# Performance work log

Measured on AMD Instinct MI355X. Metric: run time of the kernel, lower is better.

The kernel has to match this reference:

```python
import jax, jax.numpy as jnp
import numpy as np

N_INST, N_PERS, N_PROD = 20000, 50000, 30000
E_INST, E_PERS, E_PROD = 160000, 400000, 240000
F_IN, HID, HEADS, OUT = 128, 64, 4, 2
D = HID * HEADS  # 256
NEG_SLOPE_ATT = 0.2   # GATv2 attention leaky-relu slope
NEG_SLOPE_ACT = 0.01  # F.leaky_relu default
BN_EPS = 1e-5


def gatv2(x, src, dst, Wl, Wr, att, b, N):
    """Single-relation GATv2Conv (concat heads, add_self_loops=True)."""
    loop = jnp.arange(N, dtype=src.dtype)
    s = jnp.concatenate([src, loop])
    d = jnp.concatenate([dst, loop])
    H, C = att.shape
    hl = (x @ Wl).reshape(N, H, C)  # source transform
    hr = (x @ Wr).reshape(N, H, C)  # target transform
    e = jax.nn.leaky_relu(hl[s] + hr[d], NEG_SLOPE_ATT)        # [E,H,C]
    score = jnp.einsum('ehc,hc->eh', e, att)                   # [E,H]
    mx = jax.lax.stop_gradient(jax.ops.segment_max(score, d, num_segments=N))
    ex = jnp.exp(score - mx[d])
    den = jax.ops.segment_sum(ex, d, num_segments=N)           # [N,H]
    alpha = ex / (den[d] + 1e-16)
    out = jax.ops.segment_sum(alpha[..., None] * hl[s], d, num_segments=N)
    return out.reshape(N, H * C) + b


def batchnorm(x, g, b):
    mu = jnp.mean(x, axis=0)
    var = jnp.var(x, axis=0)
    return (x - mu) * jax.lax.rsqrt(var + BN_EPS) * g + b


def setup_inputs() -> dict:
    key = jax.random.key(0)
    ks = jax.random.split(key, 16)
    s = 0.05
    return {
        'x_inst': jax.random.normal(ks[0], (N_INST, F_IN), jnp.float32),
        'x_pers': jax.random.normal(ks[1], (N_PERS, F_IN), jnp.float32),
        'x_prod': jax.random.normal(ks[2], (N_PROD, F_IN), jnp.float32),
        'ei_inst': jax.random.randint(ks[3], (2, E_INST), 0, N_INST, jnp.int32),
        'ei_pers': jax.random.randint(ks[4], (2, E_PERS), 0, N_PERS, jnp.int32),
        'ei_prod': jax.random.randint(ks[5], (2, E_PROD), 0, N_PROD, jnp.int32),
        'Wl1': jax.random.normal(ks[6], (3, F_IN, D), jnp.float32) * s,
        'Wr1': jax.random.normal(ks[7], (3, F_IN, D), jnp.float32) * s,
        'att1': jax.random.normal(ks[8], (3, HEADS, HID), jnp.float32) * s,
        'b1': jnp.zeros((3, D), jnp.float32),
        'Wl2': jax.random.normal(ks[9], (3, D, D), jnp.float32) * s,
        'Wr2': jax.random.normal(ks[10], (3, D, D), jnp.float32) * s,
        'att2': jax.random.normal(ks[11], (3, HEADS, HID), jnp.float32) * s,
        'b2': jnp.zeros((3, D), jnp.float32),
        'bn_g': jnp.ones((3, D), jnp.float32),
        'bn_b': jnp.zeros((3, D), jnp.float32),
        'cW': jax.random.normal(ks[12], (D, OUT), jnp.float32) * s,
        'cb': jnp.zeros((OUT,), jnp.float32),
    }


def reference(x_inst, x_pers, x_prod, ei_inst, ei_pers, ei_prod,
              Wl1, Wr1, att1, b1, Wl2, Wr2, att2, b2,
              bn_g, bn_b, cW, cb):
    xs = (x_inst, x_pers, x_prod)
    eis = (ei_inst, ei_pers, ei_prod)
    outs = []
    for i in range(3):  # fixed set of node types
        x = xs[i]
        N = x.shape[0]
        src, dst = eis[i][0], eis[i][1]
        h = gatv2(x, src, dst, Wl1[i], Wr1[i], att1[i], b1[i], N)
        h = jax.nn.leaky_relu(batchnorm(h, bn_g[i], bn_b[i]), NEG_SLOPE_ACT)
        h = gatv2(h, src, dst, Wl2[i], Wr2[i], att2[i], b2[i], N)
        h = jax.nn.leaky_relu(batchnorm(h, bn_g[i], bn_b[i]), NEG_SLOPE_ACT)
        outs.append(h @ cW + cb)
    return tuple(outs)
```

## Files before the change

kernel.cpp:

```cpp
#include <hip/hip_runtime.h>

#define DFEAT 256
#define NEG_ATT 0.2f
#define NEG_ACT 0.01f
#define BN_EPS 1e-5f

typedef short bf16x8 __attribute__((ext_vector_type(8)));
typedef float f32x4 __attribute__((ext_vector_type(4)));

struct Int3 { int a[3]; };
struct Cp3 { const void* p[3]; };
struct Vp3 { void* p[3]; };
struct WJobs { const float* src[12]; unsigned short* dst[12]; int K[12]; };

__device__ __forceinline__ float lrelu(float x, float s) { return x > 0.f ? x : s * x; }

__device__ __forceinline__ unsigned short f2bf(float f) {
    union { float f; unsigned int u; } v; v.f = f;
    unsigned int u = v.u;
    unsigned int r = (u + 0x7FFFu + ((u >> 16) & 1u)) >> 16;
    return (unsigned short)r;
}
__device__ __forceinline__ float bf2f(unsigned short s) {
    union { unsigned int u; float f; } v; v.u = ((unsigned int)s) << 16;
    return v.f;
}
__device__ __forceinline__ float u_lo(unsigned u) {
    union { unsigned u; float f; } v; v.u = u << 16; return v.f;
}
__device__ __forceinline__ float u_hi(unsigned u) {
    union { unsigned u; float f; } v; v.u = u & 0xffff0000u; return v.f;
}

__global__ __launch_bounds__(256)
void hist_all_k(Cp3 dst, Int3 E, int* __restrict__ counts_all, Int3 nodeOff) {
    int t = blockIdx.y;
    int e = blockIdx.x * 256 + threadIdx.x;
    if (e >= E.a[t]) return;
    const int* dstp = (const int*)dst.p[t];
    atomicAdd(&counts_all[nodeOff.a[t] + dstp[e]], 1);
}

__global__ __launch_bounds__(256)
void scan1_all_k(const int* __restrict__ counts_all, int* __restrict__ offs_all,
                 int* __restrict__ bsums_all, Int3 N, Int3 nodeOff, Int3 bOff) {
    int t = blockIdx.y;
    if (blockIdx.x * 256 >= N.a[t]) return;
    const int* counts = counts_all + nodeOff.a[t];
    int* offs = offs_all + nodeOff.a[t] + t;
    int* bsums = bsums_all + bOff.a[t];
    __shared__ int buf[256];
    int tt = threadIdx.x;
    int i = blockIdx.x * 256 + tt;
    int v = (i < N.a[t]) ? counts[i] : 0;
    buf[tt] = v;
    __syncthreads();
    for (int off = 1; off < 256; off <<= 1) {
        int x = (tt >= off) ? buf[tt - off] : 0;
        __syncthreads();
        buf[tt] += x;
        __syncthreads();
    }
    if (i < N.a[t]) offs[i] = buf[tt];
    if (tt == 255) bsums[blockIdx.x] = buf[255];
}

__global__ __launch_bounds__(256)
void scan2_all_k(int* __restrict__ bsums_all, Int3 N, Int3 bOff) {
    int t = blockIdx.x;
    int nb = (N.a[t] + 255) / 256;
    int* bsums = bsums_all + bOff.a[t];
    __shared__ int buf[256];
    __shared__ int carry_s;
    int tt = threadIdx.x;
    if (tt == 0) carry_s = 0;
    __syncthreads();
    for (int base = 0; base < nb; base += 256) {
        int i = base + tt;
        int v = (i < nb) ? bsums[i] : 0;
        buf[tt] = v;
        __syncthreads();
        for (int off = 1; off < 256; off <<= 1) {
            int x = (tt >= off) ? buf[tt - off] : 0;
            __syncthreads();
            buf[tt] += x;
            __syncthreads();
        }
        int incl = buf[tt];
        int c = carry_s;
        if (i < nb) bsums[i] = c + incl - v;
        __syncthreads();
        if (tt == 255) carry_s = c + buf[255];
        __syncthreads();
    }
}

__global__ __launch_bounds__(256)
void scan3_all_k(int* __restrict__ offs_all, const int* __restrict__ counts_all,
                 const int* __restrict__ bsums_all, Int3 N, Int3 E,
                 Int3 nodeOff, Int3 bOff) {
    int t = blockIdx.y;
    if (blockIdx.x * 256 >= N.a[t]) return;
    int* offs = offs_all + nodeOff.a[t] + t;
    const int* counts = counts_all + nodeOff.a[t];
    const int* bsums = bsums_all + bOff.a[t];
    int i = blockIdx.x * 256 + threadIdx.x;
    if (i < N.a[t]) offs[i] = offs[i] - counts[i] + bsums[blockIdx.x];
    if (i == 0) offs[N.a[t]] = E.a[t];
}

__global__ __launch_bounds__(256)
void scatter_all_k(Cp3 src, Cp3 dst, Int3 E, const int* __restrict__ offs_all,
                   int* __restrict__ counts_all, int* __restrict__ csr_all,
                   Int3 nodeOff, Int3 edgeOff) {
    int t = blockIdx.y;
    int e = blockIdx.x * 256 + threadIdx.x;
    if (e >= E.a[t]) return;
    const int* srcp = (const int*)src.p[t];
    const int* dstp = (const int*)dst.p[t];
    const int* offs = offs_all + nodeOff.a[t] + t;
    int* cursor = counts_all + nodeOff.a[t];
    int* csr = csr_all + edgeOff.a[t];
    int d = dstp[e];
    int pos = atomicSub(&cursor[d], 1) - 1;
    csr[offs[d] + pos] = srcp[e];
}

__global__ __launch_bounds__(256)
void wcast_tr_k(WJobs jobs) {
    int j = blockIdx.z;
    int K = jobs.K[j];
    int k0 = blockIdx.y * 64;
    if (k0 >= K) return;
    int n0 = blockIdx.x * 64;
    const float* W = jobs.src[j];
    unsigned short* Bt = jobs.dst[j];
    __shared__ float tile[64][65];
    int tid = threadIdx.x;
    int tr = tid >> 4;
    int tc4 = (tid & 15) << 2;
#pragma unroll
    for (int r = 0; r < 4; ++r) {
        int k = tr + r * 16;
        float4 v = *(const float4*)(W + (size_t)(k0 + k) * 256 + n0 + tc4);
        tile[k][tc4] = v.x; tile[k][tc4 + 1] = v.y;
        tile[k][tc4 + 2] = v.z; tile[k][tc4 + 3] = v.w;
    }
    __syncthreads();
    int n = tid >> 2;
    int kc = (tid & 3) << 4;
    unsigned o[8];
#pragma unroll
    for (int q = 0; q < 8; ++q) {
        float v0 = tile[kc + 2 * q][n];
        float v1 = tile[kc + 2 * q + 1][n];
        o[q] = (unsigned)f2bf(v0) | ((unsigned)f2bf(v1) << 16);
    }
    unsigned short* dp = Bt + (size_t)(n0 + n) * K + k0 + kc;
    *(uint4*)dp = make_uint4(o[0], o[1], o[2], o[3]);
    *(uint4*)(dp + 8) = make_uint4(o[4], o[5], o[6], o[7]);
}

template<int AMODE>
__global__ __launch_bounds__(256)
void mfma_gemm_all_k(Cp3 Ap3, Cp3 Bp3, Cp3 ssP, Vp3 Cp3v, Int3 M3, int K) {
    int t = blockIdx.z;
    int M = M3.a[t];
    int bm = blockIdx.x * 128;
    if (bm >= M) return;
    const void* Ap = Ap3.p[t];
    const unsigned short* Bt = (const unsigned short*)Bp3.p[t];
    const float* ss = (const float*)ssP.p[t];
    unsigned short* C = (unsigned short*)Cp3v.p[t];
    const int LDK = 40;
    __shared__ unsigned short As[128 * LDK];
    __shared__ unsigned short Bs[128 * LDK];
    int tid = threadIdx.x;
    int bn = blockIdx.y * 128;
    int wid = tid >> 6, lane = tid & 63;
    int quad = lane >> 4, l16 = lane & 15;
    int mw = (wid & 1) * 64, nw = (wid >> 1) * 64;
    f32x4 acc[4][4] = {};
    for (int k0 = 0; k0 < K; k0 += 32) {
#pragma unroll
        for (int i = 0; i < 2; ++i) {
            int c = tid + 256 * i;
            int row = c >> 2, ko = (c & 3) * 8;
            int ra = bm + row; if (ra >= M) ra = M - 1;
            if (AMODE == 1) {
                const float* Af = (const float*)Ap;
                float4 a0 = *(const float4*)(Af + (size_t)ra * K + k0 + ko);
                float4 a1 = *(const float4*)(Af + (size_t)ra * K + k0 + ko + 4);
                ushort4 lo, hi;
                lo.x = f2bf(a0.x); lo.y = f2bf(a0.y); lo.z = f2bf(a0.z); lo.w = f2bf(a0.w);
                hi.x = f2bf(a1.x); hi.y = f2bf(a1.y); hi.z = f2bf(a1.z); hi.w = f2bf(a1.w);
                *(ushort4*)&As[row * LDK + ko] = lo;
                *(ushort4*)&As[row * LDK + ko + 4] = hi;
            } else if (AMODE == 2) {
                const unsigned short* Ab = (const unsigned short*)Ap;
                uint4 va = *(const uint4*)(Ab + (size_t)ra * K + k0 + ko);
                const unsigned* up = (const unsigned*)&va;
                float4 sc0 = *(const float4*)(ss + k0 + ko);
                float4 sc1 = *(const float4*)(ss + k0 + ko + 4);
                float4 sh0 = *(const float4*)(ss + 256 + k0 + ko);
                float4 sh1 = *(const float4*)(ss + 256 + k0 + ko + 4);
                float fv[8] = {u_lo(up[0]), u_hi(up[0]), u_lo(up[1]), u_hi(up[1]),
                               u_lo(up[2]), u_hi(up[2]), u_lo(up[3]), u_hi(up[3])};
                float scv[8] = {sc0.x, sc0.y, sc0.z, sc0.w, sc1.x, sc1.y, sc1.z, sc1.w};
                float shv[8] = {sh0.x, sh0.y, sh0.z, sh0.w, sh1.x, sh1.y, sh1.z, sh1.w};
                unsigned ov[4];
#pragma unroll
                for (int q = 0; q < 4; ++q) {
                    float v0 = fmaf(fv[2 * q], scv[2 * q], shv[2 * q]);
                    v0 = fmaxf(v0, NEG_ACT * v0);
                    float v1 = fmaf(fv[2 * q + 1], scv[2 * q + 1], shv[2 * q + 1]);
                    v1 = fmaxf(v1, NEG_ACT * v1);
                    ov[q] = (unsigned)f2bf(v0) | ((unsigned)f2bf(v1) << 16);
                }
                *(uint4*)&As[row * LDK + ko] = make_uint4(ov[0], ov[1], ov[2], ov[3]);
            } else {
                const unsigned short* Ab = (const unsigned short*)Ap;
                uint4 va = *(const uint4*)(Ab + (size_t)ra * K + k0 + ko);
                *(uint4*)&As[row * LDK + ko] = va;
            }
            uint4 vb = *(const uint4*)(Bt + (size_t)(bn + row) * K + k0 + ko);
            *(uint4*)&Bs[row * LDK + ko] = vb;
        }
        __syncthreads();
        bf16x8 af[4], bfv[4];
#pragma unroll
        for (int i = 0; i < 4; ++i)
            af[i] = *(bf16x8*)&As[(mw + 16 * i + l16) * LDK + quad * 8];
#pragma unroll
        for (int u = 0; u < 4; ++u)
            bfv[u] = *(bf16x8*)&Bs[(nw + 16 * u + l16) * LDK + quad * 8];
#pragma unroll
        for (int i = 0; i < 4; ++i)
#pragma unroll
            for (int u = 0; u < 4; ++u)
                acc[i][u] = __builtin_amdgcn_mfma_f32_16x16x32_bf16(af[i], bfv[u], acc[i][u], 0, 0, 0);
        __syncthreads();
    }
#pragma unroll
    for (int i = 0; i < 4; ++i) {
#pragma unroll
        for (int r = 0; r < 4; ++r) {
            int grow = bm + mw + 16 * i + quad * 4 + r;
            if (grow < M) {
#pragma unroll
                for (int u = 0; u < 4; ++u) {
                    int gcol = bn + nw + 16 * u + l16;
                    C[(size_t)grow * 512 + gcol] = f2bf(acc[i][u][r]);
                }
            }
        }
    }
}

__global__ __launch_bounds__(256, 8)
void gat_gather_all_k(Cp3 hl3, Cp3 offs3, Cp3 csr3, Cp3 att3, Cp3 bias3,
                      Vp3 out3, Int3 N3) {
    int t = blockIdx.z;
    int N = N3.a[t];
    int wave = (blockIdx.x * 256 + threadIdx.x) >> 6;
    int lane = threadIdx.x & 63;
    if (wave >= N) return;
    int d = wave;
    int half = lane >> 5;
    int l32 = lane & 31;
    const char* hlB = (const char*)hl3.p[t];
    const int* offs = (const int*)offs3.p[t];
    const int* csr  = (const int*)csr3.p[t];
    const float* att  = (const float*)att3.p[t];
    const float* bias = (const float*)bias3.p[t];
    unsigned short* out = (unsigned short*)out3.p[t];

    unsigned fOff = (unsigned)l32 << 4;

    float hr[8], at[8], ac[8];
    {
        uint4 u = *(const uint4*)(hlB + (((unsigned)d << 10) + 512u + fOff));
        const unsigned* up = (const unsigned*)&u;
#pragma unroll
        for (int j = 0; j < 4; ++j) { hr[2 * j] = u_lo(up[j]); hr[2 * j + 1] = u_hi(up[j]); }
        const float4* ap = (const float4*)(att + (l32 << 3));
        float4 a0 = ap[0], a1 = ap[1];
        at[0] = a0.x; at[1] = a0.y; at[2] = a0.z; at[3] = a0.w;
        at[4] = a1.x; at[5] = a1.y; at[6] = a1.z; at[7] = a1.w;
    }
#pragma unroll
    for (int j = 0; j < 8; ++j) ac[j] = 0.f;
    float lsum = 0.f;

    auto pair_update = [&](uint4 u, bool active) {
        const unsigned* up = (const unsigned*)&u;
        float h[8];
#pragma unroll
        for (int j = 0; j < 4; ++j) { h[2 * j] = u_lo(up[j]); h[2 * j + 1] = u_hi(up[j]); }
        float part = 0.f;
#pragma unroll
        for (int j = 0; j < 8; ++j) {
            float x = h[j] + hr[j];
            x = fmaxf(x, NEG_ATT * x);
            part = fmaf(x, at[j], part);
        }
        part += __shfl_xor(part, 1);
        part += __shfl_xor(part, 2);
        part += __shfl_xor(part, 4);
        float p = active ? __expf(part) : 0.f;
        lsum += p;
#pragma unroll
        for (int j = 0; j < 8; ++j) ac[j] = fmaf(p, h[j], ac[j]);
    };

    pair_update(*(const uint4*)(hlB + (((unsigned)d << 10) + fOff)), half == 0);

    int beg = offs[d];
    int deg = offs[d + 1] - beg;
    for (int base = 0; base < deg; base += 64) {
        int cnt = min(64, deg - base);
        int my = (base + lane < deg) ? csr[beg + base + lane] : d;
        for (int j = 0; j < cnt; j += 6) {
            uint4 v[3];
#pragma unroll
            for (int u = 0; u < 3; ++u) {
                int ei = j + 2 * u + half;
                int s = __shfl(my, ei & 63);
                if (j + 2 * u < cnt) v[u] = *(const uint4*)(hlB + (((unsigned)s << 10) + fOff));
            }
#pragma unroll
            for (int u = 0; u < 3; ++u)
                if (j + 2 * u < cnt) pair_update(v[u], (j + 2 * u + half) < cnt);
        }
    }

    lsum += __shfl_xor(lsum, 32);
#pragma unroll
    for (int j = 0; j < 8; ++j) ac[j] += __shfl_xor(ac[j], 32);

    if (half == 0) {
        float inv = 1.f / (lsum + 1e-16f);
        const float4* bp = (const float4*)(bias + (l32 << 3));
        float4 b0 = bp[0], b1 = bp[1];
        float bb[8] = {b0.x, b0.y, b0.z, b0.w, b1.x, b1.y, b1.z, b1.w};
        unsigned o[4];
#pragma unroll
        for (int j = 0; j < 4; ++j) {
            float v0 = fmaf(ac[2 * j], inv, bb[2 * j]);
            float v1 = fmaf(ac[2 * j + 1], inv, bb[2 * j + 1]);
            o[j] = (unsigned)f2bf(v0) | ((unsigned)f2bf(v1) << 16);
        }
        *(uint4*)((char*)out + (((unsigned)d << 9) + fOff)) = make_uint4(o[0], o[1], o[2], o[3]);
    }
}

__global__ __launch_bounds__(256)
void bn_stats_all_k(Cp3 h3, Vp3 st3, Int3 N3) {
    int t = blockIdx.y;
    const unsigned short* hp = (const unsigned short*)h3.p[t];
    float* st = (float*)st3.p[t];
    long total = (long)N3.a[t] * 256;
    int tid = threadIdx.x;
    long gt = (long)blockIdx.x * 256 + tid;
    long stride = (long)gridDim.x * 256 * 8;
    float s[8] = {0.f}, s2[8] = {0.f};
    for (long p = gt * 8; p < total; p += stride) {
        uint4 u = *(const uint4*)(hp + p);
        unsigned short* us = (unsigned short*)&u;
#pragma unroll
        for (int j = 0; j < 8; ++j) { float v = bf2f(us[j]); s[j] += v; s2[j] += v * v; }
    }
#pragma unroll
    for (int j = 0; j < 8; ++j) { s[j] += __shfl_xor(s[j], 32); s2[j] += __shfl_xor(s2[j], 32); }
    __shared__ float lds[2048];
    int wv = tid >> 6, lane = tid & 63;
    if (lane < 32) {
#pragma unroll
        for (int j = 0; j < 8; ++j) {
            lds[wv * 512 + lane * 8 + j] = s[j];
            lds[wv * 512 + 256 + lane * 8 + j] = s2[j];
        }
    }
    __syncthreads();
    for (int q = tid; q < 512; q += 256) {
        float v = lds[q] + lds[512 + q] + lds[1024 + q] + lds[1536 + q];
        atomicAdd(&st[q], v);
    }
}

__global__ __launch_bounds__(256)
void bn_finalize_all_k(Cp3 st3, const float* __restrict__ gb, const float* __restrict__ bb,
                       Vp3 ss3, Int3 N3) {
    int t = blockIdx.x;
    const float* st = (const float*)st3.p[t];
    float* ss = (float*)ss3.p[t];
    int f = threadIdx.x;
    float invN = 1.f / (float)N3.a[t];
    float mu  = st[f] * invN;
    float var = st[256 + f] * invN - mu * mu;
    float sc  = gb[t * DFEAT + f] / sqrtf(var + BN_EPS);
    ss[f] = sc;
    ss[256 + f] = bb[t * DFEAT + f] - mu * sc;
}

__global__ __launch_bounds__(256)
void bn_cls_all_k(Cp3 R3, Cp3 st3, const float* __restrict__ gb, const float* __restrict__ bb,
                  const float* __restrict__ cW, const float* __restrict__ cb,
                  Vp3 out3, Int3 N3) {
    int t = blockIdx.y;
    int N = N3.a[t];
    int wave = (blockIdx.x * 256 + threadIdx.x) >> 6;
    int lane = threadIdx.x & 63;
    if (wave >= N) return;
    const unsigned short* R = (const unsigned short*)R3.p[t];
    const float* stats = (const float*)st3.p[t];
    const float* g = gb + (size_t)t * DFEAT;
    const float* b = bb + (size_t)t * DFEAT;
    float* out = (float*)out3.p[t];
    int f4 = lane << 2;
    float invN = 1.f / (float)N;
    ushort4 u = *(const ushort4*)(R + (size_t)wave * DFEAT + f4);
    float vv[4] = {bf2f(u.x), bf2f(u.y), bf2f(u.z), bf2f(u.w)};
    float p0 = 0.f, p1 = 0.f;
#pragma unroll
    for (int j = 0; j < 4; ++j) {
        int f = f4 + j;
        float mu  = stats[f] * invN;
        float var = stats[DFEAT + f] * invN - mu * mu;
        float sc  = g[f] / sqrtf(var + BN_EPS);
        float val = lrelu((vv[j] - mu) * sc + b[f], NEG_ACT);
        float2 w = *(const float2*)(cW + (size_t)f * 2);
        p0 += val * w.x;
        p1 += val * w.y;
    }
#pragma unroll
    for (int off = 1; off < 64; off <<= 1) {
        p0 += __shfl_xor(p0, off);
        p1 += __shfl_xor(p1, off);
    }
    if (lane == 0) {
        out[(size_t)wave * 2 + 0] = p0 + cb[0];
        out[(size_t)wave * 2 + 1] = p1 + cb[1];
    }
}

extern "C" void kernel_launch(void* const* d_in, const int* in_sizes, int n_in,
                              void* d_out, int out_size, void* d_ws, size_t ws_size,
                              hipStream_t stream) {
    const float* x0 = (const float*)d_in[0];
    const float* x1 = (const float*)d_in[1];
    const float* x2 = (const float*)d_in[2];
    const int* ei[3] = {(const int*)d_in[3], (const int*)d_in[4], (const int*)d_in[5]};
    const float* Wl1 = (const float*)d_in[6];
    const float* Wr1 = (const float*)d_in[7];
    const float* att1 = (const float*)d_in[8];
    const float* b1 = (const float*)d_in[9];
    const float* Wl2 = (const float*)d_in[10];
    const float* Wr2 = (const float*)d_in[11];
    const float* att2 = (const float*)d_in[12];
    const float* b2 = (const float*)d_in[13];
    const float* bn_g = (const float*)d_in[14];
    const float* bn_b = (const float*)d_in[15];
    const float* cW = (const float*)d_in[16];
    const float* cb = (const float*)d_in[17];

    Int3 N3, E3, nodeOff, edgeOff, bOff;
    N3.a[0] = in_sizes[0] / 128; N3.a[1] = in_sizes[1] / 128; N3.a[2] = in_sizes[2] / 128;
    E3.a[0] = in_sizes[3] / 2;   E3.a[1] = in_sizes[4] / 2;   E3.a[2] = in_sizes[5] / 2;
    int Ntot = 0, Etot = 0, btot = 0;
    int maxN = 0, maxE = 0;
    for (int i = 0; i < 3; ++i) {
        nodeOff.a[i] = Ntot; edgeOff.a[i] = Etot; bOff.a[i] = btot;
        Ntot += N3.a[i]; Etot += E3.a[i]; btot += (N3.a[i] + 255) / 256;
        if (N3.a[i] > maxN) maxN = N3.a[i];
        if (E3.a[i] > maxE) maxE = E3.a[i];
    }

    char* w = (char*)d_ws;
    auto alloc_b = [&](size_t bytes) -> void* {
        void* p = (void*)w;
        w += (bytes + 255) & ~(size_t)255;
        return p;
    };
    unsigned short* C_all  = (unsigned short*)alloc_b((size_t)Ntot * 512 * sizeof(unsigned short));
    unsigned short* Rb_all = (unsigned short*)alloc_b((size_t)Ntot * DFEAT * sizeof(unsigned short));
    unsigned short* Bt1 = (unsigned short*)alloc_b((size_t)3 * 512 * 128 * sizeof(unsigned short));
    unsigned short* Bt2 = (unsigned short*)alloc_b((size_t)3 * 512 * 256 * sizeof(unsigned short));
    int* counts_all = (int*)alloc_b((size_t)Ntot * sizeof(int));
    int* offs_all   = (int*)alloc_b((size_t)(Ntot + 3) * sizeof(int));
    int* csr_all    = (int*)alloc_b((size_t)Etot * sizeof(int));
    int* bsums_all  = (int*)alloc_b((size_t)btot * sizeof(int));
    float* stats_all = (float*)alloc_b((size_t)6 * 512 * sizeof(float));
    float* ss_all    = (float*)alloc_b((size_t)3 * 512 * sizeof(float));

    Cp3 srcP, dstP, xP, Bt1P, Bt2P, hlP, offsP, csrP, att1P, att2P, b1P, b2P;
    Cp3 RbCP, st1CP, st2CP, ssCP, dumP;
    Vp3 CP, RbP, st1P, st2P, ssP, outP;
    for (int i = 0; i < 3; ++i) {
        srcP.p[i] = ei[i];
        dstP.p[i] = ei[i] + E3.a[i];
        xP.p[i] = (i == 0) ? (const void*)x0 : (i == 1) ? (const void*)x1 : (const void*)x2;
        Bt1P.p[i] = Bt1 + (size_t)i * 512 * 128;
        Bt2P.p[i] = Bt2 + (size_t)i * 512 * 256;
        CP.p[i] = C_all + (size_t)nodeOff.a[i] * 512;
        hlP.p[i] = CP.p[i];
        RbP.p[i] = Rb_all + (size_t)nodeOff.a[i] * DFEAT;
        RbCP.p[i] = RbP.p[i];
        offsP.p[i] = offs_all + nodeOff.a[i] + i;
        csrP.p[i] = csr_all + edgeOff.a[i];
        att1P.p[i] = att1 + (size_t)i * DFEAT;
        att2P.p[i] = att2 + (size_t)i * DFEAT;
        b1P.p[i] = b1 + (size_t)i * DFEAT;
        b2P.p[i] = b2 + (size_t)i * DFEAT;
        st1P.p[i] = stats_all + (size_t)i * 512;
        st2P.p[i] = stats_all + (size_t)(3 + i) * 512;
        st1CP.p[i] = st1P.p[i];
        st2CP.p[i] = st2P.p[i];
        ssP.p[i] = ss_all + (size_t)i * 512;
        ssCP.p[i] = ssP.p[i];
        dumP.p[i] = xP.p[i];
        outP.p[i] = (float*)d_out + (size_t)nodeOff.a[i] * 2;
    }

    int maxNblk = (maxN + 255) / 256;
    int maxEblk = (maxE + 255) / 256;
    int maxMtile = (maxN + 127) / 128;
    int maxNwave = (maxN + 3) / 4;

    hipMemsetAsync(counts_all, 0, (size_t)Ntot * sizeof(int), stream);
    hipMemsetAsync(stats_all, 0, (size_t)6 * 512 * sizeof(float), stream);
    {
        WJobs jobs;
        for (int i = 0; i < 3; ++i) {
            jobs.src[i * 4 + 0] = Wl1 + (size_t)i * 128 * 256;
            jobs.dst[i * 4 + 0] = (unsigned short*)Bt1P.p[i];
            jobs.K[i * 4 + 0] = 128;
            jobs.src[i * 4 + 1] = Wr1 + (size_t)i * 128 * 256;
            jobs.dst[i * 4 + 1] = (unsigned short*)Bt1P.p[i] + (size_t)256 * 128;
            jobs.K[i * 4 + 1] = 128;
            jobs.src[i * 4 + 2] = Wl2 + (size_t)i * 256 * 256;
            jobs.dst[i * 4 + 2] = (unsigned short*)Bt2P.p[i];
            jobs.K[i * 4 + 2] = 256;
            jobs.src[i * 4 + 3] = Wr2 + (size_t)i * 256 * 256;
            jobs.dst[i * 4 + 3] = (unsigned short*)Bt2P.p[i] + (size_t)256 * 256;
            jobs.K[i * 4 + 3] = 256;
        }
        wcast_tr_k<<<dim3(4, 4, 12), 256, 0, stream>>>(jobs);
    }

    hist_all_k<<<dim3(maxEblk, 3), 256, 0, stream>>>(dstP, E3, counts_all, nodeOff);
    scan1_all_k<<<dim3(maxNblk, 3), 256, 0, stream>>>(counts_all, offs_all, bsums_all, N3, nodeOff, bOff);
    scan2_all_k<<<3, 256, 0, stream>>>(bsums_all, N3, bOff);
    scan3_all_k<<<dim3(maxNblk, 3), 256, 0, stream>>>(offs_all, counts_all, bsums_all, N3, E3, nodeOff, bOff);
    scatter_all_k<<<dim3(maxEblk, 3), 256, 0, stream>>>(srcP, dstP, E3, offs_all, counts_all, csr_all, nodeOff, edgeOff);

    mfma_gemm_all_k<1><<<dim3(maxMtile, 4, 3), 256, 0, stream>>>(xP, Bt1P, dumP, CP, N3, 128);
    gat_gather_all_k<<<dim3(maxNwave, 1, 3), 256, 0, stream>>>(hlP, offsP, csrP, att1P, b1P, RbP, N3);
    bn_stats_all_k<<<dim3(512, 3), 256, 0, stream>>>(RbCP, st1P, N3);
    bn_finalize_all_k<<<3, 256, 0, stream>>>(st1CP, bn_g, bn_b, ssP, N3);

    mfma_gemm_all_k<2><<<dim3(maxMtile, 4, 3), 256, 0, stream>>>(RbCP, Bt2P, ssCP, CP, N3, 256);
    gat_gather_all_k<<<dim3(maxNwave, 1, 3), 256, 0, stream>>>(hlP, offsP, csrP, att2P, b2P, RbP, N3);
    bn_stats_all_k<<<dim3(512, 3), 256, 0, stream>>>(RbCP, st2P, N3);

    bn_cls_all_k<<<dim3(maxNwave, 3), 256, 0, stream>>>(RbCP, st2CP, bn_g, bn_b, cW, cb, outP, N3);
}
```

Baseline: 642.3 us.

## Map one edge per full wave with 4 features per lane in GAT gather

The GATv2 gather kernel now handles one edge per full wave, each lane covering 4 bf16 features with 8-byte loads. Before, each half-wave handled its own edge with 16-byte loads. Neighbour loads are batched 8 at a time, with a separate masked tail, instead of 3 pair-loads. The aim is more loads in flight, less half-wave masking at the tail, and no cross-half reduction at the end. The cost is an extra shuffle step in the per-head reduction and narrower memory transactions per lane; dropping the occupancy hint from launch bounds may also change register allocation.

```diff
diff --git a/kernel.cpp b/kernel.cpp
--- a/kernel.cpp
+++ b/kernel.cpp
@@ -257,7 +257,7 @@
     }
 }
 
-__global__ __launch_bounds__(256, 8)
+__global__ __launch_bounds__(256)
 void gat_gather_all_k(Cp3 hl3, Cp3 offs3, Cp3 csr3, Cp3 att3, Cp3 bias3,
                       Vp3 out3, Int3 N3) {
     int t = blockIdx.z;
@@ -265,93 +265,79 @@
     int wave = (blockIdx.x * 256 + threadIdx.x) >> 6;
     int lane = threadIdx.x & 63;
     if (wave >= N) return;
-    int d = wave;
-    int half = lane >> 5;
-    int l32 = lane & 31;
     const char* hlB = (const char*)hl3.p[t];
     const int* offs = (const int*)offs3.p[t];
-    const int* csr  = (const int*)csr3.p[t];
-    const float* att  = (const float*)att3.p[t];
+    const int* csr = (const int*)csr3.p[t];
+    const float* att = (const float*)att3.p[t];
     const float* bias = (const float*)bias3.p[t];
     unsigned short* out = (unsigned short*)out3.p[t];
-
-    unsigned fOff = (unsigned)l32 << 4;
-
-    float hr[8], at[8], ac[8];
-    {
-        uint4 u = *(const uint4*)(hlB + (((unsigned)d << 10) + 512u + fOff));
-        const unsigned* up = (const unsigned*)&u;
-#pragma unroll
-        for (int j = 0; j < 4; ++j) { hr[2 * j] = u_lo(up[j]); hr[2 * j + 1] = u_hi(up[j]); }
-        const float4* ap = (const float4*)(att + (l32 << 3));
-        float4 a0 = ap[0], a1 = ap[1];
-        at[0] = a0.x; at[1] = a0.y; at[2] = a0.z; at[3] = a0.w;
-        at[4] = a1.x; at[5] = a1.y; at[6] = a1.z; at[7] = a1.w;
-    }
-#pragma unroll
-    for (int j = 0; j < 8; ++j) ac[j] = 0.f;
-    float lsum = 0.f;
-
-    auto pair_update = [&](uint4 u, bool active) {
-        const unsigned* up = (const unsigned*)&u;
-        float h[8];
-#pragma unroll
-        for (int j = 0; j < 4; ++j) { h[2 * j] = u_lo(up[j]); h[2 * j + 1] = u_hi(up[j]); }
-        float part = 0.f;
-#pragma unroll
-        for (int j = 0; j < 8; ++j) {
-            float x = h[j] + hr[j];
-            x = fmaxf(x, NEG_ATT * x);
-            part = fmaf(x, at[j], part);
-        }
+    int d = wave;
+    unsigned lOff = (unsigned)lane << 3;
+    ushort4 hru = *(const ushort4*)(hlB + (((unsigned)d << 10) + 512u + lOff));
+    float hr0 = bf2f(hru.x), hr1 = bf2f(hru.y), hr2 = bf2f(hru.z), hr3 = bf2f(hru.w);
+    float4 av  = *(const float4*)(att + (lane << 2));
+    float4 bv  = *(const float4*)(bias + (lane << 2));
+    float l = 0.f, ac0 = 0.f, ac1 = 0.f, ac2 = 0.f, ac3 = 0.f;
+
+    auto update = [&](ushort4 u) {
+        float h0 = bf2f(u.x), h1 = bf2f(u.y), h2 = bf2f(u.z), h3 = bf2f(u.w);
+        float x0 = h0 + hr0; x0 = fmaxf(x0, NEG_ATT * x0);
+        float x1 = h1 + hr1; x1 = fmaxf(x1, NEG_ATT * x1);
+        float x2 = h2 + hr2; x2 = fmaxf(x2, NEG_ATT * x2);
+        float x3 = h3 + hr3; x3 = fmaxf(x3, NEG_ATT * x3);
+        float part = x0 * av.x;
+        part = fmaf(x1, av.y, part);
+        part = fmaf(x2, av.z, part);
+        part = fmaf(x3, av.w, part);
         part += __shfl_xor(part, 1);
         part += __shfl_xor(part, 2);
         part += __shfl_xor(part, 4);
-        float p = active ? __expf(part) : 0.f;
-        lsum += p;
-#pragma unroll
-        for (int j = 0; j < 8; ++j) ac[j] = fmaf(p, h[j], ac[j]);
+        part += __shfl_xor(part, 8);
+        float p = __expf(part);
+        l += p;
+        ac0 = fmaf(p, h0, ac0); ac1 = fmaf(p, h1, ac1);
+        ac2 = fmaf(p, h2, ac2); ac3 = fmaf(p, h3, ac3);
     };
 
-    pair_update(*(const uint4*)(hlB + (((unsigned)d << 10) + fOff)), half == 0);
+    update(*(const ushort4*)(hlB + (((unsigned)d << 10) + lOff)));
 
     int beg = offs[d];
     int deg = offs[d + 1] - beg;
     for (int base = 0; base < deg; base += 64) {
         int cnt = min(64, deg - base);
         int my = (base + lane < deg) ? csr[beg + base + lane] : d;
-        for (int j = 0; j < cnt; j += 6) {
-            uint4 v[3];
-#pragma unroll
-            for (int u = 0; u < 3; ++u) {
-                int ei = j + 2 * u + half;
-                int s = __shfl(my, ei & 63);
-                if (j + 2 * u < cnt) v[u] = *(const uint4*)(hlB + (((unsigned)s << 10) + fOff));
+        int full = cnt & ~7;
+        int j = 0;
+        for (; j < full; j += 8) {
+            ushort4 v[8];
+#pragma unroll
+            for (int u = 0; u < 8; ++u) {
+                int s = __shfl(my, j + u);
+                v[u] = *(const ushort4*)(hlB + (((unsigned)s << 10) + lOff));
             }
 #pragma unroll
-            for (int u = 0; u < 3; ++u)
-                if (j + 2 * u < cnt) pair_update(v[u], (j + 2 * u + half) < cnt);
-        }
-    }
-
-    lsum += __shfl_xor(lsum, 32);
-#pragma unroll
-    for (int j = 0; j < 8; ++j) ac[j] += __shfl_xor(ac[j], 32);
-
-    if (half == 0) {
-        float inv = 1.f / (lsum + 1e-16f);
-        const float4* bp = (const float4*)(bias + (l32 << 3));
-        float4 b0 = bp[0], b1 = bp[1];
-        float bb[8] = {b0.x, b0.y, b0.z, b0.w, b1.x, b1.y, b1.z, b1.w};
-        unsigned o[4];
-#pragma unroll
-        for (int j = 0; j < 4; ++j) {
-            float v0 = fmaf(ac[2 * j], inv, bb[2 * j]);
-            float v1 = fmaf(ac[2 * j + 1], inv, bb[2 * j + 1]);
-            o[j] = (unsigned)f2bf(v0) | ((unsigned)f2bf(v1) << 16);
-        }
-        *(uint4*)((char*)out + (((unsigned)d << 9) + fOff)) = make_uint4(o[0], o[1], o[2], o[3]);
-    }
+            for (int u = 0; u < 8; ++u) update(v[u]);
+        }
+        if (j < cnt) {
+            int kk = cnt - j;
+            ushort4 v[8];
+#pragma unroll
+            for (int u = 0; u < 8; ++u) {
+                int s = __shfl(my, (j + u) & 63);
+                if (u < kk) v[u] = *(const ushort4*)(hlB + (((unsigned)s << 10) + lOff));
+            }
+#pragma unroll
+            for (int u = 0; u < 8; ++u)
+                if (u < kk) update(v[u]);
+        }
+    }
+    float inv = 1.f / (l + 1e-16f);
+    ushort4 o;
+    o.x = f2bf(fmaf(ac0, inv, bv.x));
+    o.y = f2bf(fmaf(ac1, inv, bv.y));
+    o.z = f2bf(fmaf(ac2, inv, bv.z));
+    o.w = f2bf(fmaf(ac3, inv, bv.w));
+    *(ushort4*)((char*)out + (((unsigned)d << 9) + lOff)) = o;
 }
 
 __global__ __launch_bounds__(256)
```

Result: faster. 607.8 us (-5.4%).
